# Kernel tuning notes

Hardware: AMD Instinct MI355X
Metric: run time of the kernel (lower is better)

## Reference

```python
import jax, jax.numpy as jnp
import numpy as np

NEG_BIG = -1.0e10
LRELU_SLOPE = 0.2
N_NODES = 256  # hardcoded in the original via np.identity(256)


def setup_inputs() -> dict:
    key = jax.random.key(0)
    ks = jax.random.split(key, 7)
    B, N, F, H, F_ = 128, N_NODES, 512, 8, 64
    X = jax.random.normal(ks[0], (B, N, F), dtype=jnp.float32)
    # binary adjacency mask in {0,1}
    A = jax.random.randint(ks[1], (B, N, N), 0, 2).astype(jnp.float32)
    kernels = jax.random.normal(ks[2], (H, F, F_), dtype=jnp.float32) * 0.05
    biases = jax.random.normal(ks[3], (H, F_), dtype=jnp.float32) * 0.05
    attn_self = jax.random.normal(ks[4], (H, F_), dtype=jnp.float32) * 0.05
    attn_neigh = jax.random.normal(ks[5], (H, F_), dtype=jnp.float32) * 0.05
    alpha = jax.random.normal(ks[6], (N // 2, N // 2), dtype=jnp.float32) * 0.05
    return {"X": X, "A": A, "kernels": kernels, "biases": biases,
            "attn_self": attn_self, "attn_neigh": attn_neigh, "alpha": alpha}


def reference(X, A, kernels, biases, attn_self, attn_neigh, alpha):
    B, N, F = X.shape
    H, _, F_ = kernels.shape
    # per-head linear projection: [H,B,N,F_]
    feats = jnp.einsum('bnf,hfk->hbnk', X, kernels)
    # additive attention logits
    a_self = jnp.einsum('hbnk,hk->hbn', feats, attn_self)    # [H,B,N]
    a_neigh = jnp.einsum('hbnk,hk->hbn', feats, attn_neigh)  # [H,B,N]
    dense = a_self[..., :, None] + a_neigh[..., None, :]     # [H,B,N,N]
    dense = jnp.where(dense > 0, dense, LRELU_SLOPE * dense)  # LeakyReLU(0.2)
    dense = dense + NEG_BIG * (1.0 - A)                      # mask non-edges
    attn = jax.nn.softmax(dense, axis=-1)                    # [H,B,N,N]
    # weighted aggregation + bias (dropout is identity at inference)
    node = jnp.einsum('hbij,hbjk->hbik', attn, feats) + biases[:, None, None, :]
    # concat heads -> [B,N,H*F_], then activation (relu)
    output = jnp.transpose(node, (1, 2, 0, 3)).reshape(B, N, H * F_)
    output = jax.nn.relu(output)

    # head-averaged attention map
    view = jnp.mean(attn, axis=0)                            # [B,N,N]
    # 2x2 max pool, stride 2
    pooled = view.reshape(B, N // 2, 2, N // 2, 2).max(axis=(2, 4))  # [B,N/2,N/2]
    temp = jnp.einsum('bij,jk->bik', pooled, alpha)
    s = jnp.sum(temp, axis=(-1, -2)).reshape(B, 1)           # [B,1]
    thresh = jax.nn.sigmoid(s)                               # [B,1]
    # binarize: where((view + I) < thresh, 1, 0), per-batch scalar threshold
    eye = jnp.eye(N, dtype=view.dtype)
    dense4 = jnp.where(view + eye[None] < thresh[:, :, None],
                       jnp.ones_like(view), jnp.zeros_like(view))
    return (output, dense4)
```

## Files before the change

kernel.cpp:

```cpp
#include <hip/hip_runtime.h>
#include <hip/hip_bf16.h>
#include <cstdio>
#include <math.h>


typedef __attribute__((ext_vector_type(8))) short   s16x8;
typedef __attribute__((ext_vector_type(8))) __bf16  bf16x8;
typedef __attribute__((ext_vector_type(4))) float   fx4;

#define FADD __fadd_rn
#define FMUL __fmul_rn
#define FSUB __fsub_rn
#define FDIV __fdiv_rn
#define MASKC (-9999998976.0f)

__device__ __forceinline__ fx4 mfma_bf16_16x16x32(s16x8 a, s16x8 b, fx4 c) {
    return __builtin_amdgcn_mfma_f32_16x16x32_bf16(
        __builtin_bit_cast(bf16x8, a), __builtin_bit_cast(bf16x8, b), c, 0, 0, 0);
}
__device__ __forceinline__ unsigned short f2bf(float f) {
    unsigned int x = __builtin_bit_cast(unsigned int, f);
    unsigned int lsb = (x >> 16) & 1u;
    x += 0x7fffu + lsb;
    return (unsigned short)(x >> 16);
}
__device__ __forceinline__ float expf_cr(float x) {
    return (float)exp((double)x);
}

__device__ float pw128(const float* a) {
    float c[16];
#pragma unroll
    for (int l = 0; l < 16; ++l) {
        float t0 = FADD(FADD(a[l], a[16 + l]), FADD(a[32 + l], a[48 + l]));
        float t1 = FADD(FADD(a[64 + l], a[80 + l]), FADD(a[96 + l], a[112 + l]));
        c[l] = FADD(t0, t1);
    }
    float d[8], e[4], f[2];
#pragma unroll
    for (int l = 0; l < 8; ++l) d[l] = FADD(c[l], c[l + 8]);
#pragma unroll
    for (int l = 0; l < 4; ++l) e[l] = FADD(d[l], d[l + 4]);
#pragma unroll
    for (int l = 0; l < 2; ++l) f[l] = FADD(e[l], e[l + 2]);
    return FADD(f[0], f[1]);
}

__global__ __launch_bounds__(256) void repack_k32(const float* __restrict__ kern,
                                                  float* __restrict__ kern_r) {
    int t = blockIdx.x * 256 + threadIdx.x;
    int kk = t & 7, f = (t >> 3) & 511, kgh = t >> 12;
    int kg = kgh & 7, h = kgh >> 3;
    kern_r[t] = kern[(h * 512 + f) * 64 + kg * 8 + kk];
}

#define FCH6 64
#define XS6_STRIDE 68
__global__ __launch_bounds__(512) void feats32_emu6(const float* __restrict__ X,
                                                    const float* __restrict__ kern_r,
                                                    float* __restrict__ feats32) {
    __shared__ alignas(16) float Xs[2][64 * XS6_STRIDE];
    const int tid = threadIdx.x;
    const int hg = blockIdx.x >> 9;
    const int rb = blockIdx.x & 511;
    const int h0 = hg * 2;
    const int lane = tid & 63;
    const int kg = __builtin_amdgcn_readfirstlane(tid >> 6);
    const int k0 = kg * 8;
    const int row0 = rb * 64;
    const int srow = tid >> 3, sseg = tid & 7;

    float acc[2][8][4];
#pragma unroll
    for (int hh = 0; hh < 2; ++hh)
#pragma unroll
        for (int q = 0; q < 8; ++q)
#pragma unroll
            for (int l = 0; l < 4; ++l) acc[hh][q][l] = 0.f;

    const float* __restrict__ kp0 = &kern_r[(((h0 + 0) * 8 + kg) * 512) * 8];
    const float* __restrict__ kp1 = &kern_r[(((h0 + 1) * 8 + kg) * 512) * 8];

    {
        const float* gp = &X[(row0 + srow) * 512 + sseg * 8];
        *(float4*)&Xs[0][srow * XS6_STRIDE + sseg * 8]     = *(const float4*)gp;
        *(float4*)&Xs[0][srow * XS6_STRIDE + sseg * 8 + 4] = *(const float4*)(gp + 4);
    }
    __syncthreads();

    for (int ch = 0; ch < 8; ++ch) {
        const int fc = ch * FCH6;
        const int cur = ch & 1;
        float4 nx0, nx1;
        if (ch < 7) {
            const float* gp = &X[(row0 + srow) * 512 + fc + FCH6 + sseg * 8];
            nx0 = *(const float4*)gp;
            nx1 = *(const float4*)(gp + 4);
        }

        const float* __restrict__ xrow = &Xs[cur][lane * XS6_STRIDE];
        for (int fo = 0; fo < FCH6; fo += 8) {
            float xv[8];
            {
                float4 xa = *(const float4*)&xrow[fo];
                float4 xb = *(const float4*)&xrow[fo + 4];
                xv[0] = xa.x; xv[1] = xa.y; xv[2] = xa.z; xv[3] = xa.w;
                xv[4] = xb.x; xv[5] = xb.y; xv[6] = xb.z; xv[7] = xb.w;
            }
#pragma unroll
            for (int hh = 0; hh < 2; ++hh) {
                const float* __restrict__ kp = (hh == 0 ? kp0 : kp1) + (fc + fo) * 8;
                float w[8][8];
#pragma unroll
                for (int j = 0; j < 8; ++j) {
                    float4 lo = *(const float4*)&kp[j * 8];
                    float4 hi = *(const float4*)&kp[j * 8 + 4];
                    w[j][0] = lo.x; w[j][1] = lo.y; w[j][2] = lo.z; w[j][3] = lo.w;
                    w[j][4] = hi.x; w[j][5] = hi.y; w[j][6] = hi.z; w[j][7] = hi.w;
                }
#pragma unroll
                for (int q = 0; q < 8; ++q) {
                    acc[hh][q][0] = FADD(acc[hh][q][0], FMUL(xv[0], w[0][q]));
                    acc[hh][q][1] = FADD(acc[hh][q][1], FMUL(xv[1], w[1][q]));
                    acc[hh][q][2] = FADD(acc[hh][q][2], FMUL(xv[2], w[2][q]));
                    acc[hh][q][3] = FADD(acc[hh][q][3], FMUL(xv[3], w[3][q]));
                    acc[hh][q][0] = FADD(acc[hh][q][0], FMUL(xv[4], w[4][q]));
                    acc[hh][q][1] = FADD(acc[hh][q][1], FMUL(xv[5], w[5][q]));
                    acc[hh][q][2] = FADD(acc[hh][q][2], FMUL(xv[6], w[6][q]));
                    acc[hh][q][3] = FADD(acc[hh][q][3], FMUL(xv[7], w[7][q]));
                }
            }
        }

        if (ch < 7) {
            *(float4*)&Xs[cur ^ 1][srow * XS6_STRIDE + sseg * 8]     = nx0;
            *(float4*)&Xs[cur ^ 1][srow * XS6_STRIDE + sseg * 8 + 4] = nx1;
        }
        __syncthreads();
    }

#pragma unroll
    for (int hh = 0; hh < 2; ++hh) {
        float* __restrict__ op = &feats32[((h0 + hh) * 32768 + row0 + lane) * 64 + k0];
        float4 o0, o1;
        o0.x = FADD(FADD(acc[hh][0][0], acc[hh][0][1]), FADD(acc[hh][0][2], acc[hh][0][3]));
        o0.y = FADD(FADD(acc[hh][1][0], acc[hh][1][1]), FADD(acc[hh][1][2], acc[hh][1][3]));
        o0.z = FADD(FADD(acc[hh][2][0], acc[hh][2][1]), FADD(acc[hh][2][2], acc[hh][2][3]));
        o0.w = FADD(FADD(acc[hh][3][0], acc[hh][3][1]), FADD(acc[hh][3][2], acc[hh][3][3]));
        o1.x = FADD(FADD(acc[hh][4][0], acc[hh][4][1]), FADD(acc[hh][4][2], acc[hh][4][3]));
        o1.y = FADD(FADD(acc[hh][5][0], acc[hh][5][1]), FADD(acc[hh][5][2], acc[hh][5][3]));
        o1.z = FADD(FADD(acc[hh][6][0], acc[hh][6][1]), FADD(acc[hh][6][2], acc[hh][6][3]));
        o1.w = FADD(FADD(acc[hh][7][0], acc[hh][7][1]), FADD(acc[hh][7][2], acc[hh][7][3]));
        *(float4*)&op[0] = o0;
        *(float4*)&op[4] = o1;
    }
}

__global__ __launch_bounds__(256) void feats_to_bf(const float* __restrict__ feats32,
                                                   unsigned short* __restrict__ feats_bf) {
    int t = blockIdx.x * 256 + threadIdx.x;
    int e = t * 4;
    int k = e & 63, row = (e >> 6) & 32767, h = e >> 21;
    float4 v = *(const float4*)&feats32[e];
    ushort4 o;
    o.x = f2bf(v.x); o.y = f2bf(v.y); o.z = f2bf(v.z); o.w = f2bf(v.w);
    *(ushort4*)&feats_bf[(row << 9) + (h << 6) + k] = o;
}

__device__ float sse_dot64(const float* __restrict__ x, const float* __restrict__ y) {
    float a0 = 0.f, a1 = 0.f, a2 = 0.f, a3 = 0.f;
    for (int i = 0; i < 64; i += 8) {
        a0 = FADD(a0, FMUL(x[i + 0], y[i + 0]));
        a1 = FADD(a1, FMUL(x[i + 1], y[i + 1]));
        a2 = FADD(a2, FMUL(x[i + 2], y[i + 2]));
        a3 = FADD(a3, FMUL(x[i + 3], y[i + 3]));
        a0 = FADD(a0, FMUL(x[i + 4], y[i + 4]));
        a1 = FADD(a1, FMUL(x[i + 5], y[i + 5]));
        a2 = FADD(a2, FMUL(x[i + 6], y[i + 6]));
        a3 = FADD(a3, FMUL(x[i + 7], y[i + 7]));
    }
    return FADD(FADD(a0, a1), FADD(a2, a3));
}

__global__ __launch_bounds__(256) void logits_emu(const float* __restrict__ feats32,
                                                  const float* __restrict__ attn_s,
                                                  const float* __restrict__ attn_n,
                                                  float* __restrict__ a_s32,
                                                  float* __restrict__ a_n32) {
    int t = blockIdx.x * 256 + threadIdx.x;
    int row = t & 32767, h = t >> 15;
    const float* fr = &feats32[(h * 32768 + row) * 64];
    a_s32[h * 32768 + row] = sse_dot64(fr, &attn_s[h * 64]);
    a_n32[h * 32768 + row] = sse_dot64(fr, &attn_n[h * 64]);
}

#define VT_STRIDE 264
__global__ __launch_bounds__(256) void attn_emu(const float* __restrict__ A,
                                                const unsigned short* __restrict__ feats_bf,
                                                const float* __restrict__ a_s32,
                                                const float* __restrict__ a_n32,
                                                const float* __restrict__ biases,
                                                float* __restrict__ out0,
                                                float* __restrict__ view32) {
    __shared__ alignas(16) unsigned short Vt[64 * VT_STRIDE];
    __shared__ alignas(16) unsigned int   Abits[64][8];
    __shared__ alignas(16) float an_l[8][256];
    __shared__ alignas(16) float as_l[8][64];

    const int tid = threadIdx.x;
    const int b = blockIdx.x >> 2;
    const int row0 = (blockIdx.x & 3) * 64;
    const int w = tid >> 6, lane = tid & 63;
    const int m = lane & 15, jq = lane >> 4;

    {
        int i = tid >> 2, sg = tid & 3;
        const float* ar = &A[(((b << 8) + row0 + i) << 8) + sg * 64];
        unsigned int w0 = 0, w1 = 0;
#pragma unroll
        for (int q = 0; q < 8; ++q) {
            float4 av = *(const float4*)&ar[q * 4];
            unsigned int m4 = (av.x != 0.f ? 1u : 0u) | (av.y != 0.f ? 2u : 0u) |
                              (av.z != 0.f ? 4u : 0u) | (av.w != 0.f ? 8u : 0u);
            w0 |= m4 << (q * 4);
        }
#pragma unroll
        for (int q = 8; q < 16; ++q) {
            float4 av = *(const float4*)&ar[q * 4];
            unsigned int m4 = (av.x != 0.f ? 1u : 0u) | (av.y != 0.f ? 2u : 0u) |
                              (av.z != 0.f ? 4u : 0u) | (av.w != 0.f ? 8u : 0u);
            w1 |= m4 << ((q - 8) * 4);
        }
        Abits[i][sg * 2]     = w0;
        Abits[i][sg * 2 + 1] = w1;
    }
    for (int idx = tid; idx < 2048; idx += 256) {
        int h = idx >> 8, j = idx & 255;
        an_l[h][j] = a_n32[h * 32768 + (b << 8) + j];
    }
    for (int idx = tid; idx < 512; idx += 256) {
        int h = idx >> 6, i = idx & 63;
        as_l[h][i] = a_s32[h * 32768 + (b << 8) + row0 + i];
    }
    __syncthreads();

    const int i_ln = w * 16 + m;
    const int myrow = row0 + i_ln;
    unsigned int abits[8];
#pragma unroll
    for (int u = 0; u < 8; ++u) abits[u] = Abits[i_ln][u];

    float view_acc[8][8] = {};

    for (int h = 0; h < 8; ++h) {
        __syncthreads();
        {
            int jb = w;
#pragma unroll
            for (int it = 0; it < 8; ++it) {
                int j  = jb * 64 + it * 8 + (lane >> 3);
                int kg = lane & 7;
                s16x8 v8 = *(const s16x8*)&feats_bf[(((b << 8) + j) << 9) + (h << 6) + kg * 8];
#pragma unroll
                for (int u = 0; u < 8; ++u)
                    Vt[(kg * 8 + u) * VT_STRIDE + j] = (unsigned short)v8[u];
            }
        }
        __syncthreads();

        const float asv = as_l[h][i_ln];

        float ev[8][8];
        float Mloc = -3.4e38f;
#pragma unroll
        for (int kb = 0; kb < 8; ++kb) {
            int jbase = kb * 32 + jq * 8;
            float4 an0 = *(const float4*)&an_l[h][jbase];
            float4 an1 = *(const float4*)&an_l[h][jbase + 4];
            float anv[8] = { an0.x, an0.y, an0.z, an0.w, an1.x, an1.y, an1.z, an1.w };
            unsigned int mb = (abits[kb] >> (jq * 8)) & 0xffu;
#pragma unroll
            for (int t = 0; t < 8; ++t) {
                float lg = FADD(asv, anv[t]);
                float lr = lg > 0.f ? lg : FMUL(0.2f, lg);
                float v  = (mb & (1u << t)) ? lr : FADD(lr, MASKC);
                ev[kb][t] = v;
                Mloc = fmaxf(Mloc, v);
            }
        }
        Mloc = fmaxf(Mloc, __shfl_xor(Mloc, 16, 64));
        Mloc = fmaxf(Mloc, __shfl_xor(Mloc, 32, 64));
        const float Mi = Mloc;

#pragma unroll
        for (int kb = 0; kb < 8; ++kb)
#pragma unroll
            for (int t = 0; t < 8; ++t)
                ev[kb][t] = expf_cr(FSUB(ev[kb][t], Mi));

        float blkS[2];
#pragma unroll
        for (int blk = 0; blk < 2; ++blk) {
            float d[8];
#pragma unroll
            for (int t = 0; t < 8; ++t) {
                float s0 = FADD(ev[blk * 4 + 0][t], __shfl_xor(ev[blk * 4 + 0][t], 32, 64));
                float s1 = FADD(ev[blk * 4 + 1][t], __shfl_xor(ev[blk * 4 + 1][t], 32, 64));
                float s2 = FADD(ev[blk * 4 + 2][t], __shfl_xor(ev[blk * 4 + 2][t], 32, 64));
                float s3 = FADD(ev[blk * 4 + 3][t], __shfl_xor(ev[blk * 4 + 3][t], 32, 64));
                float cc = FADD(FADD(s0, s1), FADD(s2, s3));
                d[t] = FADD(cc, __shfl_xor(cc, 16, 64));
            }
            float e4[4], f2[2];
#pragma unroll
            for (int t = 0; t < 4; ++t) e4[t] = FADD(d[t], d[t + 4]);
            f2[0] = FADD(e4[0], e4[2]);
            f2[1] = FADD(e4[1], e4[3]);
            blkS[blk] = FADD(f2[0], f2[1]);
        }
        const float Si = FADD(blkS[0], blkS[1]);

        s16x8 pfrag[8];
#pragma unroll
        for (int kb = 0; kb < 8; ++kb) {
            s16x8 pf;
#pragma unroll
            for (int t = 0; t < 8; ++t) {
                float p = FDIV(ev[kb][t], Si);
                view_acc[kb][t] = FADD(view_acc[kb][t], FMUL(p, 0.125f));
                pf[t] = (short)f2bf(p);
            }
            pfrag[kb] = pf;
        }

        fx4 acc[4] = {};
#pragma unroll
        for (int kb = 0; kb < 8; ++kb) {
            int jo = kb * 32 + jq * 8;
#pragma unroll
            for (int nf = 0; nf < 4; ++nf) {
                s16x8 vf = *(const s16x8*)&Vt[(nf * 16 + m) * VT_STRIDE + jo];
                acc[nf] = mfma_bf16_16x16x32(pfrag[kb], vf, acc[nf]);
            }
        }
#pragma unroll
        for (int nf = 0; nf < 4; ++nf) {
            float bias = biases[h * 64 + nf * 16 + m];
#pragma unroll
            for (int r = 0; r < 4; ++r) {
                float val = acc[nf][r] + bias;
                val = val > 0.f ? val : 0.f;
                int gi = (b << 8) + row0 + w * 16 + jq * 4 + r;
                out0[gi * 512 + h * 64 + nf * 16 + m] = val;
            }
        }
    }

#pragma unroll
    for (int kb = 0; kb < 8; ++kb) {
        int base = (((b << 8) + myrow) << 8) + kb * 32 + jq * 8;
        float4 v0, v1;
        v0.x = view_acc[kb][0]; v0.y = view_acc[kb][1]; v0.z = view_acc[kb][2]; v0.w = view_acc[kb][3];
        v1.x = view_acc[kb][4]; v1.y = view_acc[kb][5]; v1.z = view_acc[kb][6]; v1.w = view_acc[kb][7];
        *(float4*)&view32[base]     = v0;
        *(float4*)&view32[base + 4] = v1;
    }
}

__global__ __launch_bounds__(256) void pool_emu(const float* __restrict__ view32,
                                                float* __restrict__ pooled) {
    int t = blockIdx.x * 256 + threadIdx.x;
    int j = t & 127, i = (t >> 7) & 127, b = t >> 14;
    const float* p = &view32[(b << 16) + (2 * i) * 256 + 2 * j];
    pooled[t] = fmaxf(fmaxf(p[0], p[1]), fmaxf(p[256], p[257]));
}

__global__ __launch_bounds__(256) void temp_emu(const float* __restrict__ pooled,
                                                const float* __restrict__ alpha,
                                                float* __restrict__ temp) {
    int t = blockIdx.x * 256 + threadIdx.x;
    int k = t & 127, i = (t >> 7) & 127, b = t >> 14;
    const float* pr = &pooled[(b << 14) + i * 128];
    const float* ap = &alpha[k];
    float a0 = 0.f, a1 = 0.f, a2 = 0.f, a3 = 0.f;
    for (int j = 0; j < 128; j += 8) {
        a0 = FADD(a0, FMUL(pr[j + 0], ap[(j + 0) * 128]));
        a1 = FADD(a1, FMUL(pr[j + 1], ap[(j + 1) * 128]));
        a2 = FADD(a2, FMUL(pr[j + 2], ap[(j + 2) * 128]));
        a3 = FADD(a3, FMUL(pr[j + 3], ap[(j + 3) * 128]));
        a0 = FADD(a0, FMUL(pr[j + 4], ap[(j + 4) * 128]));
        a1 = FADD(a1, FMUL(pr[j + 5], ap[(j + 5) * 128]));
        a2 = FADD(a2, FMUL(pr[j + 6], ap[(j + 6) * 128]));
        a3 = FADD(a3, FMUL(pr[j + 7], ap[(j + 7) * 128]));
    }
    temp[t] = FADD(FADD(a0, a1), FADD(a2, a3));
}

__global__ __launch_bounds__(128) void thresh_emu(const float* __restrict__ temp,
                                                  float* __restrict__ thresh32) {
    __shared__ float red[128];
    int l = threadIdx.x, b = blockIdx.x;
    red[l] = pw128(&temp[(b << 14) + l * 128]);
    __syncthreads();
    for (int s = 64; s >= 1; s >>= 1) {
        float v = 0.f;
        if (l < s) v = FADD(red[2 * l], red[2 * l + 1]);
        __syncthreads();
        if (l < s) red[l] = v;
        __syncthreads();
    }
    if (l == 0) {
        float sfin = red[0];
        float e = expf_cr(-sfin);
        thresh32[b] = FDIV(1.0f, FADD(1.0f, e));
    }
}

__global__ __launch_bounds__(256) void binarize_emu(const float* __restrict__ view32,
                                                    const float* __restrict__ thresh32,
                                                    float* __restrict__ out1) {
    int g = blockIdx.x * 256 + threadIdx.x;
    int e = g * 4;
    int b = e >> 16, i = (e >> 8) & 255, j = e & 255;
    float th = thresh32[b];
    float4 v = *(const float4*)&view32[e];
    float4 o;
    o.x = (FADD(v.x, (i == j + 0) ? 1.f : 0.f) < th) ? 1.f : 0.f;
    o.y = (FADD(v.y, (i == j + 1) ? 1.f : 0.f) < th) ? 1.f : 0.f;
    o.z = (FADD(v.z, (i == j + 2) ? 1.f : 0.f) < th) ? 1.f : 0.f;
    o.w = (FADD(v.w, (i == j + 3) ? 1.f : 0.f) < th) ? 1.f : 0.f;
    *(float4*)&out1[e] = o;
}

static inline void ck_launch(const char* name) {
    hipError_t e = hipGetLastError();
    if (e != hipSuccess)
        fprintf(stderr, "[gat] %s launch error %d: %s\n", name, (int)e, hipGetErrorString(e));
}

extern "C" void kernel_launch(void* const* d_in, const int* in_sizes, int n_in,
                              void* d_out, int out_size, void* d_ws, size_t ws_size,
                              hipStream_t stream) {
    const float* X      = (const float*)d_in[0];
    const float* A      = (const float*)d_in[1];
    const float* kern   = (const float*)d_in[2];
    const float* biases = (const float*)d_in[3];
    const float* attn_s = (const float*)d_in[4];
    const float* attn_n = (const float*)d_in[5];
    const float* alpha  = (const float*)d_in[6];

    char* ws = (char*)d_ws;
    unsigned short* feats_bf = (unsigned short*)(ws);
    float*          feats32  = (float*)(ws + 33554432);
    float*          view32   = (float*)(ws + 100663296);
    float*          a_s32    = (float*)(ws + 134217728);
    float*          a_n32    = (float*)(ws + 135266304);
    float*          pooled   = (float*)(ws + 136314880);
    float*          temp     = (float*)(ws + 144703488);
    float*          thresh32 = (float*)(ws + 153092096);

    float*          kern_r   = (float*)(ws + 100663296);

    float* out0 = (float*)d_out;
    float* out1 = out0 + 16777216;

    repack_k32  <<<1024, 256, 0, stream>>>(kern, kern_r);           ck_launch("repack_k32");
    feats32_emu6<<<2048, 512, 0, stream>>>(X, kern_r, feats32);     ck_launch("feats32_emu6");
    feats_to_bf <<<16384, 256, 0, stream>>>(feats32, feats_bf);     ck_launch("feats_to_bf");
    logits_emu  <<<1024, 256, 0, stream>>>(feats32, attn_s, attn_n, a_s32, a_n32);
                                                                    ck_launch("logits_emu");
    attn_emu    <<<512, 256, 0, stream>>>(A, feats_bf, a_s32, a_n32, biases, out0, view32);
                                                                    ck_launch("attn_emu");
    pool_emu    <<<8192, 256, 0, stream>>>(view32, pooled);         ck_launch("pool_emu");
    temp_emu    <<<8192, 256, 0, stream>>>(pooled, alpha, temp);    ck_launch("temp_emu");
    thresh_emu  <<<128, 128, 0, stream>>>(temp, thresh32);          ck_launch("thresh_emu");
    binarize_emu<<<8192, 256, 0, stream>>>(view32, thresh32, out1); ck_launch("binarize_emu");
}
```

Before: 625.9 us.

## Pre-transpose bf16 features per head so attention reads V fragments from global

The bf16 conversion kernel now writes features in a per-(batch,head) transposed layout [k][j], going through an LDS tile to do the transpose. The attention kernel drops its per-head LDS staging of V and the two barriers around it, and loads MFMA B-fragments straight from global memory. This removes the strided LDS scatter and the block synchronisations in the head loop. In exchange, V fragments are re-read from global/L2 by every wave and every row block.

```diff
diff --git a/kernel.cpp b/kernel.cpp
--- a/kernel.cpp
+++ b/kernel.cpp
@@ -23,6 +23,9 @@
     unsigned int lsb = (x >> 16) & 1u;
     x += 0x7fffu + lsb;
     return (unsigned short)(x >> 16);
+}
+__device__ __forceinline__ unsigned int pack2(float a, float b) {
+    return (unsigned int)f2bf(a) | ((unsigned int)f2bf(b) << 16);
 }
 __device__ __forceinline__ float expf_cr(float x) {
     return (float)exp((double)x);
@@ -156,15 +159,37 @@
     }
 }
 
-__global__ __launch_bounds__(256) void feats_to_bf(const float* __restrict__ feats32,
-                                                   unsigned short* __restrict__ feats_bf) {
-    int t = blockIdx.x * 256 + threadIdx.x;
-    int e = t * 4;
-    int k = e & 63, row = (e >> 6) & 32767, h = e >> 21;
-    float4 v = *(const float4*)&feats32[e];
-    ushort4 o;
-    o.x = f2bf(v.x); o.y = f2bf(v.y); o.z = f2bf(v.z); o.w = f2bf(v.w);
-    *(ushort4*)&feats_bf[(row << 9) + (h << 6) + k] = o;
+#define TS 74
+__global__ __launch_bounds__(256) void feats_to_bfT(const float* __restrict__ feats32,
+                                                    unsigned short* __restrict__ feats_bfT) {
+    __shared__ unsigned short Ts[64 * TS];
+    const int tid = threadIdx.x;
+    const int jblk = blockIdx.x & 3;
+    const int b = (blockIdx.x >> 2) & 127;
+    const int h = blockIdx.x >> 9;
+    {
+        int jl = tid >> 2, seg = tid & 3;
+        int row = b * 256 + jblk * 64 + jl;
+        const float* src = &feats32[(h * 32768 + row) * 64 + seg * 16];
+        unsigned short* dst = &Ts[jl * TS + seg * 16];
+#pragma unroll
+        for (int u = 0; u < 4; ++u) {
+            float4 v = *(const float4*)&src[u * 4];
+            *(unsigned int*)&dst[u * 4]     = pack2(v.x, v.y);
+            *(unsigned int*)&dst[u * 4 + 2] = pack2(v.z, v.w);
+        }
+    }
+    __syncthreads();
+    {
+        int kl = tid >> 2, js = tid & 3;
+        unsigned short tmp[16];
+#pragma unroll
+        for (int u = 0; u < 16; ++u)
+            tmp[u] = Ts[(js * 16 + u) * TS + kl];
+        unsigned short* out = &feats_bfT[((b * 8 + h) * 64 + kl) * 256 + jblk * 64 + js * 16];
+        *(s16x8*)&out[0] = *(s16x8*)&tmp[0];
+        *(s16x8*)&out[8] = *(s16x8*)&tmp[8];
+    }
 }
 
 __device__ float sse_dot64(const float* __restrict__ x, const float* __restrict__ y) {
@@ -194,15 +219,13 @@
     a_n32[h * 32768 + row] = sse_dot64(fr, &attn_n[h * 64]);
 }
 
-#define VT_STRIDE 264
 __global__ __launch_bounds__(256) void attn_emu(const float* __restrict__ A,
-                                                const unsigned short* __restrict__ feats_bf,
+                                                const unsigned short* __restrict__ feats_bfT,
                                                 const float* __restrict__ a_s32,
                                                 const float* __restrict__ a_n32,
                                                 const float* __restrict__ biases,
                                                 float* __restrict__ out0,
                                                 float* __restrict__ view32) {
-    __shared__ alignas(16) unsigned short Vt[64 * VT_STRIDE];
     __shared__ alignas(16) unsigned int   Abits[64][8];
     __shared__ alignas(16) float an_l[8][256];
     __shared__ alignas(16) float as_l[8][64];
@@ -253,21 +276,7 @@
     float view_acc[8][8] = {};
 
     for (int h = 0; h < 8; ++h) {
-        __syncthreads();
-        {
-            int jb = w;
-#pragma unroll
-            for (int it = 0; it < 8; ++it) {
-                int j  = jb * 64 + it * 8 + (lane >> 3);
-                int kg = lane & 7;
-                s16x8 v8 = *(const s16x8*)&feats_bf[(((b << 8) + j) << 9) + (h << 6) + kg * 8];
-#pragma unroll
-                for (int u = 0; u < 8; ++u)
-                    Vt[(kg * 8 + u) * VT_STRIDE + j] = (unsigned short)v8[u];
-            }
-        }
-        __syncthreads();
-
+        const unsigned short* __restrict__ vbase = &feats_bfT[(b * 8 + h) << 14];
         const float asv = as_l[h][i_ln];
 
         float ev[8][8];
@@ -339,7 +348,7 @@
             int jo = kb * 32 + jq * 8;
 #pragma unroll
             for (int nf = 0; nf < 4; ++nf) {
-                s16x8 vf = *(const s16x8*)&Vt[(nf * 16 + m) * VT_STRIDE + jo];
+                s16x8 vf = *(const s16x8*)&vbase[((nf * 16 + m) << 8) + jo];
                 acc[nf] = mfma_bf16_16x16x32(pfrag[kb], vf, acc[nf]);
             }
         }
@@ -450,7 +459,7 @@
     const float* alpha  = (const float*)d_in[6];
 
     char* ws = (char*)d_ws;
-    unsigned short* feats_bf = (unsigned short*)(ws);
+    unsigned short* feats_bfT = (unsigned short*)(ws);
     float*          feats32  = (float*)(ws + 33554432);
     float*          view32   = (float*)(ws + 100663296);
     float*          a_s32    = (float*)(ws + 134217728);
@@ -464,15 +473,15 @@
     float* out0 = (float*)d_out;
     float* out1 = out0 + 16777216;
 
-    repack_k32  <<<1024, 256, 0, stream>>>(kern, kern_r);           ck_launch("repack_k32");
-    feats32_emu6<<<2048, 512, 0, stream>>>(X, kern_r, feats32);     ck_launch("feats32_emu6");
-    feats_to_bf <<<16384, 256, 0, stream>>>(feats32, feats_bf);     ck_launch("feats_to_bf");
-    logits_emu  <<<1024, 256, 0, stream>>>(feats32, attn_s, attn_n, a_s32, a_n32);
+    repack_k32   <<<1024, 256, 0, stream>>>(kern, kern_r);          ck_launch("repack_k32");
+    feats32_emu6 <<<2048, 512, 0, stream>>>(X, kern_r, feats32);    ck_launch("feats32_emu6");
+    feats_to_bfT <<<4096, 256, 0, stream>>>(feats32, feats_bfT);    ck_launch("feats_to_bfT");
+    logits_emu   <<<1024, 256, 0, stream>>>(feats32, attn_s, attn_n, a_s32, a_n32);
                                                                     ck_launch("logits_emu");
-    attn_emu    <<<512, 256, 0, stream>>>(A, feats_bf, a_s32, a_n32, biases, out0, view32);
+    attn_emu     <<<512, 256, 0, stream>>>(A, feats_bfT, a_s32, a_n32, biases, out0, view32);
                                                                     ck_launch("attn_emu");
-    pool_emu    <<<8192, 256, 0, stream>>>(view32, pooled);         ck_launch("pool_emu");
-    temp_emu    <<<8192, 256, 0, stream>>>(pooled, alpha, temp);    ck_launch("temp_emu");
-    thresh_emu  <<<128, 128, 0, stream>>>(temp, thresh32);          ck_launch("thresh_emu");
-    binarize_emu<<<8192, 256, 0, stream>>>(view32, thresh32, out1); ck_launch("binarize_emu");
-}
+    pool_emu     <<<8192, 256, 0, stream>>>(view32, pooled);        ck_launch("pool_emu");
+    temp_emu     <<<8192, 256, 0, stream>>>(pooled, alpha, temp);   ck_launch("temp_emu");
+    thresh_emu   <<<128, 128, 0, stream>>>(temp, thresh32);         ck_launch("thresh_emu");
+    binarize_emu <<<8192, 256, 0, stream>>>(view32, thresh32, out1);ck_launch("binarize_emu");
+}
```

Measured after the change: 679.5 us. +8.6%, slower.

## Fuse bf16 conversion and attention logits into the feature projection epilogue

Applied to the files above, without the earlier changes.

The projection kernel now converts its fp32 results to bf16 itself and computes the self and neighbour attention logits from a shared-memory staging copy. This removes the separate conversion and logits kernels along with the fp32 feats buffer write and its two re-reads. The bf16 feature layout changes to head-major, so the attention kernel's gather address is updated to match. The epilogue adds a shared-memory round trip and a barrier, and only half the threads do the logit dot products.

```diff
diff --git a/kernel.cpp b/kernel.cpp
--- a/kernel.cpp
+++ b/kernel.cpp
@@ -44,127 +44,6 @@
 #pragma unroll
     for (int l = 0; l < 2; ++l) f[l] = FADD(e[l], e[l + 2]);
     return FADD(f[0], f[1]);
-}
-
-__global__ __launch_bounds__(256) void repack_k32(const float* __restrict__ kern,
-                                                  float* __restrict__ kern_r) {
-    int t = blockIdx.x * 256 + threadIdx.x;
-    int kk = t & 7, f = (t >> 3) & 511, kgh = t >> 12;
-    int kg = kgh & 7, h = kgh >> 3;
-    kern_r[t] = kern[(h * 512 + f) * 64 + kg * 8 + kk];
-}
-
-#define FCH6 64
-#define XS6_STRIDE 68
-__global__ __launch_bounds__(512) void feats32_emu6(const float* __restrict__ X,
-                                                    const float* __restrict__ kern_r,
-                                                    float* __restrict__ feats32) {
-    __shared__ alignas(16) float Xs[2][64 * XS6_STRIDE];
-    const int tid = threadIdx.x;
-    const int hg = blockIdx.x >> 9;
-    const int rb = blockIdx.x & 511;
-    const int h0 = hg * 2;
-    const int lane = tid & 63;
-    const int kg = __builtin_amdgcn_readfirstlane(tid >> 6);
-    const int k0 = kg * 8;
-    const int row0 = rb * 64;
-    const int srow = tid >> 3, sseg = tid & 7;
-
-    float acc[2][8][4];
-#pragma unroll
-    for (int hh = 0; hh < 2; ++hh)
-#pragma unroll
-        for (int q = 0; q < 8; ++q)
-#pragma unroll
-            for (int l = 0; l < 4; ++l) acc[hh][q][l] = 0.f;
-
-    const float* __restrict__ kp0 = &kern_r[(((h0 + 0) * 8 + kg) * 512) * 8];
-    const float* __restrict__ kp1 = &kern_r[(((h0 + 1) * 8 + kg) * 512) * 8];
-
-    {
-        const float* gp = &X[(row0 + srow) * 512 + sseg * 8];
-        *(float4*)&Xs[0][srow * XS6_STRIDE + sseg * 8]     = *(const float4*)gp;
-        *(float4*)&Xs[0][srow * XS6_STRIDE + sseg * 8 + 4] = *(const float4*)(gp + 4);
-    }
-    __syncthreads();
-
-    for (int ch = 0; ch < 8; ++ch) {
-        const int fc = ch * FCH6;
-        const int cur = ch & 1;
-        float4 nx0, nx1;
-        if (ch < 7) {
-            const float* gp = &X[(row0 + srow) * 512 + fc + FCH6 + sseg * 8];
-            nx0 = *(const float4*)gp;
-            nx1 = *(const float4*)(gp + 4);
-        }
-
-        const float* __restrict__ xrow = &Xs[cur][lane * XS6_STRIDE];
-        for (int fo = 0; fo < FCH6; fo += 8) {
-            float xv[8];
-            {
-                float4 xa = *(const float4*)&xrow[fo];
-                float4 xb = *(const float4*)&xrow[fo + 4];
-                xv[0] = xa.x; xv[1] = xa.y; xv[2] = xa.z; xv[3] = xa.w;
-                xv[4] = xb.x; xv[5] = xb.y; xv[6] = xb.z; xv[7] = xb.w;
-            }
-#pragma unroll
-            for (int hh = 0; hh < 2; ++hh) {
-                const float* __restrict__ kp = (hh == 0 ? kp0 : kp1) + (fc + fo) * 8;
-                float w[8][8];
-#pragma unroll
-                for (int j = 0; j < 8; ++j) {
-                    float4 lo = *(const float4*)&kp[j * 8];
-                    float4 hi = *(const float4*)&kp[j * 8 + 4];
-                    w[j][0] = lo.x; w[j][1] = lo.y; w[j][2] = lo.z; w[j][3] = lo.w;
-                    w[j][4] = hi.x; w[j][5] = hi.y; w[j][6] = hi.z; w[j][7] = hi.w;
-                }
-#pragma unroll
-                for (int q = 0; q < 8; ++q) {
-                    acc[hh][q][0] = FADD(acc[hh][q][0], FMUL(xv[0], w[0][q]));
-                    acc[hh][q][1] = FADD(acc[hh][q][1], FMUL(xv[1], w[1][q]));
-                    acc[hh][q][2] = FADD(acc[hh][q][2], FMUL(xv[2], w[2][q]));
-                    acc[hh][q][3] = FADD(acc[hh][q][3], FMUL(xv[3], w[3][q]));
-                    acc[hh][q][0] = FADD(acc[hh][q][0], FMUL(xv[4], w[4][q]));
-                    acc[hh][q][1] = FADD(acc[hh][q][1], FMUL(xv[5], w[5][q]));
-                    acc[hh][q][2] = FADD(acc[hh][q][2], FMUL(xv[6], w[6][q]));
-                    acc[hh][q][3] = FADD(acc[hh][q][3], FMUL(xv[7], w[7][q]));
-                }
-            }
-        }
-
-        if (ch < 7) {
-            *(float4*)&Xs[cur ^ 1][srow * XS6_STRIDE + sseg * 8]     = nx0;
-            *(float4*)&Xs[cur ^ 1][srow * XS6_STRIDE + sseg * 8 + 4] = nx1;
-        }
-        __syncthreads();
-    }
-
-#pragma unroll
-    for (int hh = 0; hh < 2; ++hh) {
-        float* __restrict__ op = &feats32[((h0 + hh) * 32768 + row0 + lane) * 64 + k0];
-        float4 o0, o1;
-        o0.x = FADD(FADD(acc[hh][0][0], acc[hh][0][1]), FADD(acc[hh][0][2], acc[hh][0][3]));
-        o0.y = FADD(FADD(acc[hh][1][0], acc[hh][1][1]), FADD(acc[hh][1][2], acc[hh][1][3]));
-        o0.z = FADD(FADD(acc[hh][2][0], acc[hh][2][1]), FADD(acc[hh][2][2], acc[hh][2][3]));
-        o0.w = FADD(FADD(acc[hh][3][0], acc[hh][3][1]), FADD(acc[hh][3][2], acc[hh][3][3]));
-        o1.x = FADD(FADD(acc[hh][4][0], acc[hh][4][1]), FADD(acc[hh][4][2], acc[hh][4][3]));
-        o1.y = FADD(FADD(acc[hh][5][0], acc[hh][5][1]), FADD(acc[hh][5][2], acc[hh][5][3]));
-        o1.z = FADD(FADD(acc[hh][6][0], acc[hh][6][1]), FADD(acc[hh][6][2], acc[hh][6][3]));
-        o1.w = FADD(FADD(acc[hh][7][0], acc[hh][7][1]), FADD(acc[hh][7][2], acc[hh][7][3]));
-        *(float4*)&op[0] = o0;
-        *(float4*)&op[4] = o1;
-    }
-}
-
-__global__ __launch_bounds__(256) void feats_to_bf(const float* __restrict__ feats32,
-                                                   unsigned short* __restrict__ feats_bf) {
-    int t = blockIdx.x * 256 + threadIdx.x;
-    int e = t * 4;
-    int k = e & 63, row = (e >> 6) & 32767, h = e >> 21;
-    float4 v = *(const float4*)&feats32[e];
-    ushort4 o;
-    o.x = f2bf(v.x); o.y = f2bf(v.y); o.z = f2bf(v.z); o.w = f2bf(v.w);
-    *(ushort4*)&feats_bf[(row << 9) + (h << 6) + k] = o;
 }
 
 __device__ float sse_dot64(const float* __restrict__ x, const float* __restrict__ y) {
@@ -182,16 +61,135 @@
     return FADD(FADD(a0, a1), FADD(a2, a3));
 }
 
-__global__ __launch_bounds__(256) void logits_emu(const float* __restrict__ feats32,
-                                                  const float* __restrict__ attn_s,
-                                                  const float* __restrict__ attn_n,
-                                                  float* __restrict__ a_s32,
-                                                  float* __restrict__ a_n32) {
+__global__ __launch_bounds__(256) void repack_k32(const float* __restrict__ kern,
+                                                  float* __restrict__ kern_r) {
     int t = blockIdx.x * 256 + threadIdx.x;
-    int row = t & 32767, h = t >> 15;
-    const float* fr = &feats32[(h * 32768 + row) * 64];
-    a_s32[h * 32768 + row] = sse_dot64(fr, &attn_s[h * 64]);
-    a_n32[h * 32768 + row] = sse_dot64(fr, &attn_n[h * 64]);
+    int kk = t & 7, f = (t >> 3) & 511, kgh = t >> 12;
+    int kg = kgh & 7, h = kgh >> 3;
+    kern_r[t] = kern[(h * 512 + f) * 64 + kg * 8 + kk];
+}
+
+#define FCH6 64
+#define XS6_STRIDE 68
+__global__ __launch_bounds__(512) void feats32_emu7(const float* __restrict__ X,
+                                                    const float* __restrict__ kern_r,
+                                                    const float* __restrict__ attn_s,
+                                                    const float* __restrict__ attn_n,
+                                                    unsigned short* __restrict__ feats_bf,
+                                                    float* __restrict__ a_s32,
+                                                    float* __restrict__ a_n32) {
+    __shared__ alignas(16) float Xs[2][64 * XS6_STRIDE];
+    const int tid = threadIdx.x;
+    const int hg = blockIdx.x >> 9;
+    const int rb = blockIdx.x & 511;
+    const int h0 = hg * 2;
+    const int lane = tid & 63;
+    const int kg = __builtin_amdgcn_readfirstlane(tid >> 6);
+    const int k0 = kg * 8;
+    const int row0 = rb * 64;
+    const int srow = tid >> 3, sseg = tid & 7;
+
+    float acc[2][8][4];
+#pragma unroll
+    for (int hh = 0; hh < 2; ++hh)
+#pragma unroll
+        for (int q = 0; q < 8; ++q)
+#pragma unroll
+            for (int l = 0; l < 4; ++l) acc[hh][q][l] = 0.f;
+
+    const float* __restrict__ kp0 = &kern_r[(((h0 + 0) * 8 + kg) * 512) * 8];
+    const float* __restrict__ kp1 = &kern_r[(((h0 + 1) * 8 + kg) * 512) * 8];
+
+    {
+        const float* gp = &X[(row0 + srow) * 512 + sseg * 8];
+        *(float4*)&Xs[0][srow * XS6_STRIDE + sseg * 8]     = *(const float4*)gp;
+        *(float4*)&Xs[0][srow * XS6_STRIDE + sseg * 8 + 4] = *(const float4*)(gp + 4);
+    }
+    __syncthreads();
+
+    for (int ch = 0; ch < 8; ++ch) {
+        const int fc = ch * FCH6;
+        const int cur = ch & 1;
+        float4 nx0, nx1;
+        if (ch < 7) {
+            const float* gp = &X[(row0 + srow) * 512 + fc + FCH6 + sseg * 8];
+            nx0 = *(const float4*)gp;
+            nx1 = *(const float4*)(gp + 4);
+        }
+
+        const float* __restrict__ xrow = &Xs[cur][lane * XS6_STRIDE];
+        for (int fo = 0; fo < FCH6; fo += 8) {
+            float xv[8];
+            {
+                float4 xa = *(const float4*)&xrow[fo];
+                float4 xb = *(const float4*)&xrow[fo + 4];
+                xv[0] = xa.x; xv[1] = xa.y; xv[2] = xa.z; xv[3] = xa.w;
+                xv[4] = xb.x; xv[5] = xb.y; xv[6] = xb.z; xv[7] = xb.w;
+            }
+#pragma unroll
+            for (int hh = 0; hh < 2; ++hh) {
+                const float* __restrict__ kp = (hh == 0 ? kp0 : kp1) + (fc + fo) * 8;
+                float w[8][8];
+#pragma unroll
+                for (int j = 0; j < 8; ++j) {
+                    float4 lo = *(const float4*)&kp[j * 8];
+                    float4 hi = *(const float4*)&kp[j * 8 + 4];
+                    w[j][0] = lo.x; w[j][1] = lo.y; w[j][2] = lo.z; w[j][3] = lo.w;
+                    w[j][4] = hi.x; w[j][5] = hi.y; w[j][6] = hi.z; w[j][7] = hi.w;
+                }
+#pragma unroll
+                for (int q = 0; q < 8; ++q) {
+                    acc[hh][q][0] = FADD(acc[hh][q][0], FMUL(xv[0], w[0][q]));
+                    acc[hh][q][1] = FADD(acc[hh][q][1], FMUL(xv[1], w[1][q]));
+                    acc[hh][q][2] = FADD(acc[hh][q][2], FMUL(xv[2], w[2][q]));
+                    acc[hh][q][3] = FADD(acc[hh][q][3], FMUL(xv[3], w[3][q]));
+                    acc[hh][q][0] = FADD(acc[hh][q][0], FMUL(xv[4], w[4][q]));
+                    acc[hh][q][1] = FADD(acc[hh][q][1], FMUL(xv[5], w[5][q]));
+                    acc[hh][q][2] = FADD(acc[hh][q][2], FMUL(xv[6], w[6][q]));
+                    acc[hh][q][3] = FADD(acc[hh][q][3], FMUL(xv[7], w[7][q]));
+                }
+            }
+        }
+
+        if (ch < 7) {
+            *(float4*)&Xs[cur ^ 1][srow * XS6_STRIDE + sseg * 8]     = nx0;
+            *(float4*)&Xs[cur ^ 1][srow * XS6_STRIDE + sseg * 8 + 4] = nx1;
+        }
+        __syncthreads();
+    }
+
+    float* __restrict__ Ls = &Xs[0][0];
+#pragma unroll
+    for (int hh = 0; hh < 2; ++hh) {
+        float4 o0, o1;
+        o0.x = FADD(FADD(acc[hh][0][0], acc[hh][0][1]), FADD(acc[hh][0][2], acc[hh][0][3]));
+        o0.y = FADD(FADD(acc[hh][1][0], acc[hh][1][1]), FADD(acc[hh][1][2], acc[hh][1][3]));
+        o0.z = FADD(FADD(acc[hh][2][0], acc[hh][2][1]), FADD(acc[hh][2][2], acc[hh][2][3]));
+        o0.w = FADD(FADD(acc[hh][3][0], acc[hh][3][1]), FADD(acc[hh][3][2], acc[hh][3][3]));
+        o1.x = FADD(FADD(acc[hh][4][0], acc[hh][4][1]), FADD(acc[hh][4][2], acc[hh][4][3]));
+        o1.y = FADD(FADD(acc[hh][5][0], acc[hh][5][1]), FADD(acc[hh][5][2], acc[hh][5][3]));
+        o1.z = FADD(FADD(acc[hh][6][0], acc[hh][6][1]), FADD(acc[hh][6][2], acc[hh][6][3]));
+        o1.w = FADD(FADD(acc[hh][7][0], acc[hh][7][1]), FADD(acc[hh][7][2], acc[hh][7][3]));
+
+        unsigned short* bp = &feats_bf[((h0 + hh) * 32768 + row0 + lane) * 64 + k0];
+        ushort4 b0, b1;
+        b0.x = f2bf(o0.x); b0.y = f2bf(o0.y); b0.z = f2bf(o0.z); b0.w = f2bf(o0.w);
+        b1.x = f2bf(o1.x); b1.y = f2bf(o1.y); b1.z = f2bf(o1.z); b1.w = f2bf(o1.w);
+        *(ushort4*)&bp[0] = b0;
+        *(ushort4*)&bp[4] = b1;
+
+        *(float4*)&Ls[hh * (64 * XS6_STRIDE) + lane * XS6_STRIDE + k0]     = o0;
+        *(float4*)&Ls[hh * (64 * XS6_STRIDE) + lane * XS6_STRIDE + k0 + 4] = o1;
+    }
+    __syncthreads();
+    if (tid < 256) {
+        int row = tid & 63, hh = (tid >> 6) & 1, which = tid >> 7;
+        const float* xr = &Ls[hh * (64 * XS6_STRIDE) + row * XS6_STRIDE];
+        const float* vec = which ? &attn_n[(h0 + hh) * 64] : &attn_s[(h0 + hh) * 64];
+        float r = sse_dot64(xr, vec);
+        float* dst = which ? a_n32 : a_s32;
+        dst[(h0 + hh) * 32768 + row0 + row] = r;
+    }
 }
 
 #define VT_STRIDE 264
@@ -260,7 +258,7 @@
             for (int it = 0; it < 8; ++it) {
                 int j  = jb * 64 + it * 8 + (lane >> 3);
                 int kg = lane & 7;
-                s16x8 v8 = *(const s16x8*)&feats_bf[(((b << 8) + j) << 9) + (h << 6) + kg * 8];
+                s16x8 v8 = *(const s16x8*)&feats_bf[(h * 32768 + (b << 8) + j) * 64 + kg * 8];
 #pragma unroll
                 for (int u = 0; u < 8; ++u)
                     Vt[(kg * 8 + u) * VT_STRIDE + j] = (unsigned short)v8[u];
@@ -451,7 +449,6 @@
 
     char* ws = (char*)d_ws;
     unsigned short* feats_bf = (unsigned short*)(ws);
-    float*          feats32  = (float*)(ws + 33554432);
     float*          view32   = (float*)(ws + 100663296);
     float*          a_s32    = (float*)(ws + 134217728);
     float*          a_n32    = (float*)(ws + 135266304);
@@ -464,15 +461,14 @@
     float* out0 = (float*)d_out;
     float* out1 = out0 + 16777216;
 
-    repack_k32  <<<1024, 256, 0, stream>>>(kern, kern_r);           ck_launch("repack_k32");
-    feats32_emu6<<<2048, 512, 0, stream>>>(X, kern_r, feats32);     ck_launch("feats32_emu6");
-    feats_to_bf <<<16384, 256, 0, stream>>>(feats32, feats_bf);     ck_launch("feats_to_bf");
-    logits_emu  <<<1024, 256, 0, stream>>>(feats32, attn_s, attn_n, a_s32, a_n32);
-                                                                    ck_launch("logits_emu");
-    attn_emu    <<<512, 256, 0, stream>>>(A, feats_bf, a_s32, a_n32, biases, out0, view32);
+    repack_k32   <<<1024, 256, 0, stream>>>(kern, kern_r);          ck_launch("repack_k32");
+    feats32_emu7 <<<2048, 512, 0, stream>>>(X, kern_r, attn_s, attn_n,
+                                            feats_bf, a_s32, a_n32);
+                                                                    ck_launch("feats32_emu7");
+    attn_emu     <<<512, 256, 0, stream>>>(A, feats_bf, a_s32, a_n32, biases, out0, view32);
                                                                     ck_launch("attn_emu");
-    pool_emu    <<<8192, 256, 0, stream>>>(view32, pooled);         ck_launch("pool_emu");
-    temp_emu    <<<8192, 256, 0, stream>>>(pooled, alpha, temp);    ck_launch("temp_emu");
-    thresh_emu  <<<128, 128, 0, stream>>>(temp, thresh32);          ck_launch("thresh_emu");
-    binarize_emu<<<8192, 256, 0, stream>>>(view32, thresh32, out1); ck_launch("binarize_emu");
-}
+    pool_emu     <<<8192, 256, 0, stream>>>(view32, pooled);        ck_launch("pool_emu");
+    temp_emu     <<<8192, 256, 0, stream>>>(pooled, alpha, temp);   ck_launch("temp_emu");
+    thresh_emu   <<<128, 128, 0, stream>>>(temp, thresh32);         ck_launch("thresh_emu");
+    binarize_emu <<<8192, 256, 0, stream>>>(view32, thresh32, out1);ck_launch("binarize_emu");
+}
```

After: 1.651 ms. 2.64x slower.
